# Optimization experiments

Hardware: AMD Instinct MI355X
Metric: run time of the kernel (lower is better)

## Reference

```python
import jax, jax.numpy as jnp
import numpy as np

B, L, FD, G = 256, 512, 64, 32
H1, H2, DH = 512, 512, 256  # leaf_hidden=[512,512], diffuse_hidden=[256]

def _gelu(x):
    return jax.nn.gelu(x, approximate=False)  # torch nn.GELU default (erf)

def setup_inputs() -> dict:
    key = jax.random.key(0)
    ks = jax.random.split(key, 14)
    def lin(k, fan_in, shape):
        s = 1.0 / np.sqrt(fan_in)
        return jax.random.uniform(k, shape, jnp.float32, -s, s)
    return {
        "Xg": jax.random.normal(ks[0], (B, G), jnp.float32),
        "Xl": jax.random.normal(ks[1], (B, L, FD), jnp.float32),
        "W1": lin(ks[2], FD, (FD, H1)), "b1": lin(ks[3], FD, (H1,)),
        "W2": lin(ks[4], H1, (H1, H2)), "b2": lin(ks[5], H1, (H2,)),
        "wa": lin(ks[6], H2, (H2, 1)), "ba": lin(ks[7], H2, (1,)),
        "wt": lin(ks[8], H2, (H2, 1)), "bt": lin(ks[9], H2, (1,)),
        "Wd1": lin(ks[10], G + H2, (G + H2, DH)), "bd1": lin(ks[11], G + H2, (DH,)),
        "Wd2": lin(ks[12], DH, (DH, 1)), "bd2": lin(ks[13], DH, (1,)),
    }

def reference(Xg, Xl, W1, b1, W2, b2, wa, ba, wt, bt, Wd1, bd1, Wd2, bd2):
    # per-leaf MLP encoder: [B, L, FD] -> [B, L, H2]
    h = _gelu(jnp.einsum("blf,fh->blh", Xl, W1) + b1)
    h = _gelu(jnp.einsum("blh,hk->blk", h, W2) + b2)
    absorb = jax.nn.softplus(jnp.einsum("blh,ho->bl", h, wa) + ba[0])  # [B, L]
    atten = jax.nn.softplus(jnp.einsum("blh,ho->bl", h, wt) + bt[0])   # [B, L]
    # flip bottom->top to top->bottom
    absorb_tb = absorb[:, ::-1]
    atten_tb = atten[:, ::-1]
    # T_i = prod_{j<i} exp(-atten_tb_j) = exp(-exclusive_cumsum(atten_tb))
    excl = jnp.cumsum(atten_tb, axis=1) - atten_tb
    T = jnp.exp(-excl)
    captured = jnp.sum(T * absorb_tb, axis=1, keepdims=True)  # [B, 1]
    pooled = jnp.mean(h, axis=1)  # [B, H2]
    z = jnp.concatenate([Xg, pooled], axis=1)
    d = _gelu(z @ Wd1 + bd1) @ Wd2 + bd2  # [B, 1]
    return captured + d
```

## Files before the change

### kernel.cpp

```cpp
#include <hip/hip_runtime.h>
#include <hip/hip_bf16.h>
#include <math.h>

#define B_SZ   256
#define L_SZ   512
#define FD_SZ  64
#define H1_SZ  512
#define H2_SZ  512
#define G_SZ   32
#define DH_SZ  256
#define M_SZ   (B_SZ * L_SZ)

typedef __bf16 bfx8 __attribute__((ext_vector_type(8)));
typedef __bf16 bfx4 __attribute__((ext_vector_type(4)));
typedef float  f32x4 __attribute__((ext_vector_type(4)));

__device__ __forceinline__ float gelu_exact(float x) {
  return 0.5f * x * (1.0f + erff(x * 0.70710678118654752440f));
}
__device__ __forceinline__ float gelu_fast(float x) {
  float x2 = x * x;
  float v = x * fmaf(0.0713548163f, x2, 1.5957691216f);
  float e = __expf(-v);
  return x * __builtin_amdgcn_rcpf(1.0f + e);
}
__device__ __forceinline__ float softplus_f(float x) {
  return (x > 20.0f) ? x : log1pf(expf(x));
}
__device__ __forceinline__ __bf16 f2bf(float f) { return (__bf16)f; }

__device__ __forceinline__ float dpp_xor1(float x) {
  int r = __builtin_amdgcn_mov_dpp(__builtin_bit_cast(int, x), 0xB1, 0xF, 0xF, true);
  return __builtin_bit_cast(float, r);
}
__device__ __forceinline__ float dpp_xor2(float x) {
  int r = __builtin_amdgcn_mov_dpp(__builtin_bit_cast(int, x), 0x4E, 0xF, 0xF, true);
  return __builtin_bit_cast(float, r);
}

#define MFMA16(a, b, c) __builtin_amdgcn_mfma_f32_16x16x32_bf16((a), (b), (c), 0, 0, 0)

__global__ void repack_kernel(const float* __restrict__ W1,
                              const float* __restrict__ W2,
                              __bf16* __restrict__ W1p,
                              __bf16* __restrict__ W2p) {
  int t = blockIdx.x * 256 + threadIdx.x;
  if (t < 4096) {
    int lane = t & 63, blk = t >> 6;
    int ks = blk & 1, mb = blk >> 1;
    int col = 16 * mb + (lane & 15);
    int kbase = ks * 32 + (lane >> 4) * 8;
    bfx8 o;
#pragma unroll
    for (int j = 0; j < 8; ++j) o[j] = f2bf(W1[(size_t)(kbase + j) * H1_SZ + col]);
    *reinterpret_cast<bfx8*>(W1p + (size_t)t * 8) = o;
  } else if (t < 4096 + 32768) {
    int t2 = t - 4096;
    int lane = t2 & 63, blk = t2 >> 6;
    int ks = blk & 15, nb = blk >> 4;
    int col = 16 * nb + (lane & 15);
    int kbase = ks * 32 + (lane >> 4) * 8;
    bfx8 o;
#pragma unroll
    for (int j = 0; j < 8; ++j) o[j] = f2bf(W2[(size_t)(kbase + j) * H2_SZ + col]);
    *reinterpret_cast<bfx8*>(W2p + (size_t)t2 * 8) = o;
  }
}

__global__ __launch_bounds__(512, 4) void fused_kernel(
    const float* __restrict__ Xl,
    const __bf16* __restrict__ W1p, const __bf16* __restrict__ W2p,
    const float* __restrict__ b1, const float* __restrict__ b2,
    const float* __restrict__ wa, const float* __restrict__ ba,
    const float* __restrict__ wt, const float* __restrict__ bt,
    float* __restrict__ absorbW, float* __restrict__ attenW,
    float* __restrict__ pooled) {
  __shared__ __bf16 H1s[64 * 512];
  __shared__ float absorb_l[64];
  __shared__ float atten_l[64];

  const int tid = threadIdx.x;
  const int lane = tid & 63;
  const int w = tid >> 6;
  const int g = lane >> 4;
  const int c = lane & 15;
  const int R0 = blockIdx.x * 64;
  const int bidx = R0 >> 9;

  if (tid < 64) { absorb_l[tid] = 0.0f; atten_l[tid] = 0.0f; }

  f32x4 acc1[4][4];
#pragma unroll
  for (int mi = 0; mi < 4; ++mi)
#pragma unroll
    for (int ni = 0; ni < 4; ++ni) acc1[mi][ni] = (f32x4){0.f, 0.f, 0.f, 0.f};

#pragma unroll
  for (int ks = 0; ks < 2; ++ks) {
    bfx8 a1[4];
#pragma unroll
    for (int mi = 0; mi < 4; ++mi) {
      int mb = 4 * w + mi;
      a1[mi] = *reinterpret_cast<const bfx8*>(W1p + ((size_t)(mb * 2 + ks) * 64 + lane) * 8);
    }
    bfx8 bx[4];
#pragma unroll
    for (int ni = 0; ni < 4; ++ni) {
      const float* xp = Xl + (size_t)(R0 + 16 * ni + c) * FD_SZ + 32 * ks + 8 * g;
      float4 u0 = *reinterpret_cast<const float4*>(xp);
      float4 u1 = *reinterpret_cast<const float4*>(xp + 4);
      bfx8 bv;
      bv[0] = f2bf(u0.x); bv[1] = f2bf(u0.y); bv[2] = f2bf(u0.z); bv[3] = f2bf(u0.w);
      bv[4] = f2bf(u1.x); bv[5] = f2bf(u1.y); bv[6] = f2bf(u1.z); bv[7] = f2bf(u1.w);
      bx[ni] = bv;
    }
#pragma unroll
    for (int mi = 0; mi < 4; ++mi)
#pragma unroll
      for (int ni = 0; ni < 4; ++ni)
        acc1[mi][ni] = MFMA16(a1[mi], bx[ni], acc1[mi][ni]);
  }

#pragma unroll
  for (int mi = 0; mi < 4; ++mi) {
    int mb = 4 * w + mi;
    float4 bias4 = *reinterpret_cast<const float4*>(b1 + 16 * mb + 4 * g);
#pragma unroll
    for (int ni = 0; ni < 4; ++ni) {
      int r = 16 * ni + c;
      bfx4 pv;
      pv[0] = f2bf(gelu_fast(acc1[mi][ni][0] + bias4.x));
      pv[1] = f2bf(gelu_fast(acc1[mi][ni][1] + bias4.y));
      pv[2] = f2bf(gelu_fast(acc1[mi][ni][2] + bias4.z));
      pv[3] = f2bf(gelu_fast(acc1[mi][ni][3] + bias4.w));
      int kchunk = 2 * mb + (g >> 1);
      int off = r * 512 + ((kchunk ^ (r & 7)) << 3) + (g & 1) * 4;
      *reinterpret_cast<bfx4*>(&H1s[off]) = pv;
    }
  }
  __syncthreads();

  f32x4 acc2[4][4];
#pragma unroll
  for (int m = 0; m < 4; ++m)
#pragma unroll
    for (int ni = 0; ni < 4; ++ni) acc2[m][ni] = (f32x4){0.f, 0.f, 0.f, 0.f};

  for (int ks = 0; ks < 16; ++ks) {
    bfx8 a2[4];
#pragma unroll
    for (int m = 0; m < 4; ++m) {
      int r = 16 * m + c;
      int chunk = 4 * ks + g;
      a2[m] = *reinterpret_cast<const bfx8*>(&H1s[r * 512 + ((chunk ^ (r & 7)) << 3)]);
    }
    bfx8 bw[4];
#pragma unroll
    for (int ni = 0; ni < 4; ++ni) {
      int nb = 4 * w + ni;
      bw[ni] = *reinterpret_cast<const bfx8*>(W2p + ((size_t)(nb * 16 + ks) * 64 + lane) * 8);
    }
#pragma unroll
    for (int ni = 0; ni < 4; ++ni)
#pragma unroll
      for (int m = 0; m < 4; ++m)
        acc2[m][ni] = MFMA16(a2[m], bw[ni], acc2[m][ni]);
  }

  float b2v[4], wav[4], wtv[4];
#pragma unroll
  for (int ni = 0; ni < 4; ++ni) {
    int col = 16 * (4 * w + ni) + c;
    b2v[ni] = b2[col];
    wav[ni] = wa[col];
    wtv[ni] = wt[col];
  }
  float pool[4];
#pragma unroll
  for (int ni = 0; ni < 4; ++ni) pool[ni] = 0.0f;

#pragma unroll
  for (int m = 0; m < 4; ++m) {
#pragma unroll
    for (int reg = 0; reg < 4; ++reg) {
      float sa = 0.0f, st = 0.0f;
#pragma unroll
      for (int ni = 0; ni < 4; ++ni) {
        float v = gelu_fast(acc2[m][ni][reg] + b2v[ni]);
        sa += v * wav[ni];
        st += v * wtv[ni];
        pool[ni] += v;
      }
      sa += dpp_xor1(sa);  st += dpp_xor1(st);
      sa += dpp_xor2(sa);  st += dpp_xor2(st);
      sa += __shfl_xor(sa, 4, 64);  st += __shfl_xor(st, 4, 64);
      sa += __shfl_xor(sa, 8, 64);  st += __shfl_xor(st, 8, 64);
      if (c == 0) {
        int row = 16 * m + 4 * g + reg;
        atomicAdd(&absorb_l[row], sa);
        atomicAdd(&atten_l[row], st);
      }
    }
  }
#pragma unroll
  for (int ni = 0; ni < 4; ++ni) {
    float v = pool[ni];
    v += __shfl_xor(v, 16, 64);
    v += __shfl_xor(v, 32, 64);
    if (g == 0) atomicAdd(&pooled[bidx * H2_SZ + 16 * (4 * w + ni) + c], v);
  }
  __syncthreads();

  if (tid < 64) {
    absorbW[R0 + tid] = softplus_f(absorb_l[tid] + ba[0]);
    attenW[R0 + tid]  = softplus_f(atten_l[tid] + bt[0]);
  }
}

__global__ __launch_bounds__(256) void finalize_kernel(
    const float* __restrict__ Xg,
    const float* __restrict__ absorbW, const float* __restrict__ attenW,
    const float* __restrict__ pooled,
    const float* __restrict__ Wd1, const float* __restrict__ bd1,
    const float* __restrict__ Wd2, const float* __restrict__ bd2,
    float* __restrict__ out) {
  __shared__ float s0[512];
  __shared__ float s1[512];
  __shared__ float sab[512];
  __shared__ float zz[544];
  __shared__ float redc[4];
  __shared__ float redd[4];

  const int b = blockIdx.x;
  const int t = threadIdx.x;
  const int i0 = t, i1 = t + 256;

  float a0 = attenW[b * L_SZ + (L_SZ - 1 - i0)];
  float a1 = attenW[b * L_SZ + (L_SZ - 1 - i1)];
  sab[i0] = absorbW[b * L_SZ + (L_SZ - 1 - i0)];
  sab[i1] = absorbW[b * L_SZ + (L_SZ - 1 - i1)];
  s0[i0] = a0; s0[i1] = a1;
  __syncthreads();

  float* src = s0;
  float* dst = s1;
  for (int off = 1; off < 512; off <<= 1) {
    float v0 = src[i0] + ((i0 >= off) ? src[i0 - off] : 0.0f);
    float v1 = src[i1] + ((i1 >= off) ? src[i1 - off] : 0.0f);
    dst[i0] = v0; dst[i1] = v1;
    __syncthreads();
    float* tmp = src; src = dst; dst = tmp;
  }

  float p = expf(-(src[i0] - a0)) * sab[i0] + expf(-(src[i1] - a1)) * sab[i1];
#pragma unroll
  for (int off = 32; off; off >>= 1) p += __shfl_down(p, off, 64);
  if ((t & 63) == 0) redc[t >> 6] = p;

  if (t < G_SZ) zz[t] = Xg[b * G_SZ + t];
  zz[G_SZ + i0] = pooled[b * H2_SZ + i0] * (1.0f / (float)L_SZ);
  zz[G_SZ + i1] = pooled[b * H2_SZ + i1] * (1.0f / (float)L_SZ);
  __syncthreads();

  float s = bd1[t];
  for (int cc = 0; cc < G_SZ + H2_SZ; ++cc) s = fmaf(zz[cc], Wd1[cc * DH_SZ + t], s);
  float v = gelu_exact(s) * Wd2[t];
#pragma unroll
  for (int off = 32; off; off >>= 1) v += __shfl_down(v, off, 64);
  if ((t & 63) == 0) redd[t >> 6] = v;
  __syncthreads();

  if (t == 0) {
    float captured = redc[0] + redc[1] + redc[2] + redc[3];
    float d = redd[0] + redd[1] + redd[2] + redd[3] + bd2[0];
    out[b] = captured + d;
  }
}

extern "C" void kernel_launch(void* const* d_in, const int* in_sizes, int n_in,
                              void* d_out, int out_size, void* d_ws, size_t ws_size,
                              hipStream_t stream) {
  const float* Xg  = (const float*)d_in[0];
  const float* Xl  = (const float*)d_in[1];
  const float* W1  = (const float*)d_in[2];
  const float* b1  = (const float*)d_in[3];
  const float* W2  = (const float*)d_in[4];
  const float* b2  = (const float*)d_in[5];
  const float* wa  = (const float*)d_in[6];
  const float* ba  = (const float*)d_in[7];
  const float* wt  = (const float*)d_in[8];
  const float* bt  = (const float*)d_in[9];
  const float* Wd1 = (const float*)d_in[10];
  const float* bd1 = (const float*)d_in[11];
  const float* Wd2 = (const float*)d_in[12];
  const float* bd2 = (const float*)d_in[13];

  char* ws = (char*)d_ws;
  __bf16* W1p    = (__bf16*)(ws + 0);
  __bf16* W2p    = (__bf16*)(ws + 65536);
  float* absorbW = (float*)(ws + 589824);
  float* attenW  = (float*)(ws + 1114112);
  float* pooled  = (float*)(ws + 1638400);

  hipMemsetAsync(pooled, 0, B_SZ * H2_SZ * sizeof(float), stream);
  repack_kernel<<<144, 256, 0, stream>>>(W1, W2, W1p, W2p);
  fused_kernel<<<M_SZ / 64, 512, 0, stream>>>(Xl, W1p, W2p, b1, b2, wa, ba, wt, bt,
                                              absorbW, attenW, pooled);
  finalize_kernel<<<B_SZ, 256, 0, stream>>>(Xg, absorbW, attenW, pooled,
                                            Wd1, bd1, Wd2, bd2, (float*)d_out);
}
```

Measured before the change: 145.2 us.

## Prefetch W2 fragments, use row-rotate DPP reductions, replace LDS atomics with per-wave slots

The second GEMM loop is fully unrolled and double-buffers the W2 global loads one k-step ahead, so the memory latency overlaps the MFMAs. The 16-lane reductions use DPP row_ror instead of ds_swizzle shuffles. The shared-memory atomics for the absorb and atten partials are replaced by per-wave float2 slots that one wave sums after the barrier. GELU now uses exp2 with pre-scaled constants, and the H1 swizzle index takes c&7 in place of r&7. The cost is extra registers for the prefetch buffer and full unrolling, which may lower occupancy.

```diff
diff --git a/kernel.cpp b/kernel.cpp
--- a/kernel.cpp
+++ b/kernel.cpp
@@ -20,8 +20,8 @@
 }
 __device__ __forceinline__ float gelu_fast(float x) {
   float x2 = x * x;
-  float v = x * fmaf(0.0713548163f, x2, 1.5957691216f);
-  float e = __expf(-v);
+  float w = x * fmaf(0.102943398f, x2, 2.30220931f);
+  float e = __builtin_amdgcn_exp2f(-w);
   return x * __builtin_amdgcn_rcpf(1.0f + e);
 }
 __device__ __forceinline__ float softplus_f(float x) {
@@ -29,14 +29,12 @@
 }
 __device__ __forceinline__ __bf16 f2bf(float f) { return (__bf16)f; }
 
-__device__ __forceinline__ float dpp_xor1(float x) {
-  int r = __builtin_amdgcn_mov_dpp(__builtin_bit_cast(int, x), 0xB1, 0xF, 0xF, true);
-  return __builtin_bit_cast(float, r);
-}
-__device__ __forceinline__ float dpp_xor2(float x) {
-  int r = __builtin_amdgcn_mov_dpp(__builtin_bit_cast(int, x), 0x4E, 0xF, 0xF, true);
-  return __builtin_bit_cast(float, r);
-}
+#define ROR_ADD(x, n)                                                          \
+  {                                                                            \
+    int _t = __builtin_amdgcn_mov_dpp(__builtin_bit_cast(int, (x)),            \
+                                      0x120 + (n), 0xF, 0xF, true);            \
+    (x) += __builtin_bit_cast(float, _t);                                      \
+  }
 
 #define MFMA16(a, b, c) __builtin_amdgcn_mfma_f32_16x16x32_bf16((a), (b), (c), 0, 0, 0)
 
@@ -76,8 +74,7 @@
     float* __restrict__ absorbW, float* __restrict__ attenW,
     float* __restrict__ pooled) {
   __shared__ __bf16 H1s[64 * 512];
-  __shared__ float absorb_l[64];
-  __shared__ float atten_l[64];
+  __shared__ float sl[8 * 64 * 2];
 
   const int tid = threadIdx.x;
   const int lane = tid & 63;
@@ -86,8 +83,6 @@
   const int c = lane & 15;
   const int R0 = blockIdx.x * 64;
   const int bidx = R0 >> 9;
-
-  if (tid < 64) { absorb_l[tid] = 0.0f; atten_l[tid] = 0.0f; }
 
   f32x4 acc1[4][4];
 #pragma unroll
@@ -146,25 +141,36 @@
 #pragma unroll
     for (int ni = 0; ni < 4; ++ni) acc2[m][ni] = (f32x4){0.f, 0.f, 0.f, 0.f};
 
+  const __bf16* wpb = W2p + ((size_t)(4 * w) * 16 * 64 + lane) * 8;
+  bfx8 bw[4];
+#pragma unroll
+  for (int ni = 0; ni < 4; ++ni)
+    bw[ni] = *reinterpret_cast<const bfx8*>(wpb + ni * 8192);
+
+#pragma unroll
   for (int ks = 0; ks < 16; ++ks) {
     bfx8 a2[4];
 #pragma unroll
     for (int m = 0; m < 4; ++m) {
       int r = 16 * m + c;
       int chunk = 4 * ks + g;
-      a2[m] = *reinterpret_cast<const bfx8*>(&H1s[r * 512 + ((chunk ^ (r & 7)) << 3)]);
-    }
-    bfx8 bw[4];
-#pragma unroll
-    for (int ni = 0; ni < 4; ++ni) {
-      int nb = 4 * w + ni;
-      bw[ni] = *reinterpret_cast<const bfx8*>(W2p + ((size_t)(nb * 16 + ks) * 64 + lane) * 8);
+      a2[m] = *reinterpret_cast<const bfx8*>(&H1s[r * 512 + ((chunk ^ (c & 7)) << 3)]);
+    }
+    bfx8 bwn[4];
+    if (ks < 15) {
+#pragma unroll
+      for (int ni = 0; ni < 4; ++ni)
+        bwn[ni] = *reinterpret_cast<const bfx8*>(wpb + ni * 8192 + (ks + 1) * 512);
     }
 #pragma unroll
     for (int ni = 0; ni < 4; ++ni)
 #pragma unroll
       for (int m = 0; m < 4; ++m)
         acc2[m][ni] = MFMA16(a2[m], bw[ni], acc2[m][ni]);
+    if (ks < 15) {
+#pragma unroll
+      for (int ni = 0; ni < 4; ++ni) bw[ni] = bwn[ni];
+    }
   }
 
   float b2v[4], wav[4], wtv[4];
@@ -187,18 +193,16 @@
 #pragma unroll
       for (int ni = 0; ni < 4; ++ni) {
         float v = gelu_fast(acc2[m][ni][reg] + b2v[ni]);
-        sa += v * wav[ni];
-        st += v * wtv[ni];
+        sa = fmaf(v, wav[ni], sa);
+        st = fmaf(v, wtv[ni], st);
         pool[ni] += v;
       }
-      sa += dpp_xor1(sa);  st += dpp_xor1(st);
-      sa += dpp_xor2(sa);  st += dpp_xor2(st);
-      sa += __shfl_xor(sa, 4, 64);  st += __shfl_xor(st, 4, 64);
-      sa += __shfl_xor(sa, 8, 64);  st += __shfl_xor(st, 8, 64);
+      ROR_ADD(sa, 8); ROR_ADD(sa, 4); ROR_ADD(sa, 2); ROR_ADD(sa, 1);
+      ROR_ADD(st, 8); ROR_ADD(st, 4); ROR_ADD(st, 2); ROR_ADD(st, 1);
       if (c == 0) {
         int row = 16 * m + 4 * g + reg;
-        atomicAdd(&absorb_l[row], sa);
-        atomicAdd(&atten_l[row], st);
+        float2 v2 = make_float2(sa, st);
+        *reinterpret_cast<float2*>(&sl[w * 128 + row * 2]) = v2;
       }
     }
   }
@@ -212,8 +216,14 @@
   __syncthreads();
 
   if (tid < 64) {
-    absorbW[R0 + tid] = softplus_f(absorb_l[tid] + ba[0]);
-    attenW[R0 + tid]  = softplus_f(atten_l[tid] + bt[0]);
+    float sa = 0.0f, st = 0.0f;
+#pragma unroll
+    for (int w8 = 0; w8 < 8; ++w8) {
+      float2 v2 = *reinterpret_cast<float2*>(&sl[w8 * 128 + tid * 2]);
+      sa += v2.x; st += v2.y;
+    }
+    absorbW[R0 + tid] = softplus_f(sa + ba[0]);
+    attenW[R0 + tid]  = softplus_f(st + bt[0]);
   }
 }
 
```

Measured after the change: 185.7 us. 27.9% more time.
